# Optimization experiments

Hardware: AMD Instinct MI355X
Metric: run time of the kernel (lower is better)

## Reference

```python
import jax, jax.numpy as jnp
import numpy as np

B, SEQ, NV = 4, 1024, 32
PL, D, H, E_LAYERS, DFF = 16, 512, 8, 4, 2048
P = SEQ // PL  # 64 patches -> L = P*NV = 2048 tokens
WIN = 4
DH = D // H
SCALE = float(1.0 / np.sqrt(DH))


def layernorm(x, g, b):
    m = x.mean(-1, keepdims=True)
    v = jnp.var(x, axis=-1, keepdims=True)
    return (x - m) / jnp.sqrt(v + 1e-5) * g + b


def setup_inputs() -> dict:
    key = jax.random.key(0)
    ks = jax.random.split(key, 32)
    s = 0.02
    d = {}
    d['x_enc'] = jax.random.normal(ks[0], (B, SEQ, NV), jnp.float32)
    d['mask'] = jax.random.uniform(ks[1], (B, P, NV)) < 0.5  # mask_ratio=0.5
    d['W_embed'] = jax.random.normal(ks[2], (PL, D), jnp.float32) * s
    d['b_embed'] = jnp.zeros((D,), jnp.float32)
    per = lambda k, shp: jax.random.normal(k, (E_LAYERS,) + shp, jnp.float32) * s
    d['Wq'] = per(ks[3], (D, D)); d['bq'] = jnp.zeros((E_LAYERS, D))
    d['Wk'] = per(ks[4], (D, D)); d['bk'] = jnp.zeros((E_LAYERS, D))
    d['Wv'] = per(ks[5], (D, D)); d['bv'] = jnp.zeros((E_LAYERS, D))
    d['Wo'] = per(ks[6], (D, D)); d['bo'] = jnp.zeros((E_LAYERS, D))
    d['W1'] = per(ks[7], (D, DFF)); d['b1'] = jnp.zeros((E_LAYERS, DFF))
    d['W2'] = per(ks[8], (DFF, D)); d['b2'] = jnp.zeros((E_LAYERS, D))
    d['g1'] = jnp.ones((E_LAYERS, D)); d['be1'] = jnp.zeros((E_LAYERS, D))
    d['g2'] = jnp.ones((E_LAYERS, D)); d['be2'] = jnp.zeros((E_LAYERS, D))
    d['gf'] = jnp.ones((D,)); d['bf'] = jnp.zeros((D,))
    d['W_proj'] = jax.random.normal(ks[9], (D, PL), jnp.float32) * s
    d['b_proj'] = jnp.zeros((PL,), jnp.float32)
    return d


def reference(x_enc, mask, W_embed, b_embed, Wq, bq, Wk, bk, Wv, bv, Wo, bo,
              W1, b1, W2, b2, g1, be1, g2, be2, gf, bf, W_proj, b_proj):
    # instance norm over time (means detached, stdev differentiable as in torch)
    means = jax.lax.stop_gradient(x_enc.mean(1, keepdims=True))
    x = x_enc - means
    stdev = jnp.sqrt(jnp.var(x, axis=1, keepdims=True) + 1e-5)
    x = x / stdev
    # patchify: [B, P, NV, PL]
    patches = x[:, :P * PL, :].reshape(B, P, PL, NV).transpose(0, 1, 3, 2)
    emb = patches @ W_embed + b_embed                  # [B,P,NV,D]
    emb = jnp.where(mask[..., None], 0.0, emb)         # zero masked patches
    tok = emb.reshape(B, P * NV, D)                    # [B,L,D]
    # local/banded attention mask over patch index
    pid = jnp.arange(P * NV) // NV
    bad = jnp.abs(pid[:, None] - pid[None, :]) > WIN   # [L,L] True = masked
    for l in range(E_LAYERS):
        q = (tok @ Wq[l] + bq[l]).reshape(B, -1, H, DH)
        k = (tok @ Wk[l] + bk[l]).reshape(B, -1, H, DH)
        v = (tok @ Wv[l] + bv[l]).reshape(B, -1, H, DH)
        scores = jnp.einsum('blhe,bshe->bhls', q, k)
        scores = jnp.where(bad[None, None], -jnp.inf, scores)
        A = jax.nn.softmax(SCALE * scores, axis=-1)
        o = jnp.einsum('bhls,bshe->blhe', A, v).reshape(B, -1, D)
        tok = layernorm(tok + (o @ Wo[l] + bo[l]), g1[l], be1[l])
        y = jax.nn.gelu(tok @ W1[l] + b1[l], approximate=False) @ W2[l] + b2[l]
        tok = layernorm(tok + y, g2[l], be2[l])
    tok = layernorm(tok, gf, bf)
    enc = tok.reshape(B, P, NV, D)
    recon = enc @ W_proj + b_proj                      # [B,P,NV,PL]
    sc = stdev[:, 0, :][:, None, :, None]
    bi = means[:, 0, :][:, None, :, None]
    recon = recon * sc + bi
    target = patches * sc + bi
    mf = mask[..., None].astype(recon.dtype)
    denom = mf.sum() * PL
    denom = jnp.where(denom == 0, 1.0, denom)
    return (((recon - target) ** 2) * mf).sum() / denom
```

## Files before the change

### kernel.cpp

```cpp
#include <hip/hip_runtime.h>
#include <hip/hip_bf16.h>

#define DEV __device__ __forceinline__

namespace {

constexpr int Bn  = 4, SEQ = 1024, NV = 32, PL = 16, D = 512, H = 8, DFF = 2048;
constexpr int P   = SEQ / PL;
constexpr int L   = P * NV;
constexpr int M   = Bn * L;
constexpr int WIN = 4;

using short8   = __attribute__((ext_vector_type(8))) short;
using ushort8  = __attribute__((ext_vector_type(8))) unsigned short;
using float4v  = __attribute__((ext_vector_type(4))) float;

DEV float b2f(unsigned short u) { return __uint_as_float(((unsigned)u) << 16); }
DEV unsigned short f2b(float f) {
  unsigned fb = __float_as_uint(f);
  return (unsigned short)((fb + 0x7FFFu + ((fb >> 16) & 1u)) >> 16);
}
DEV unsigned short f2bt(float f) {
  return (unsigned short)(__float_as_uint(f) >> 16);
}
DEV float ldf(const void* p, size_t idx, int bf) {
  if (bf) return b2f(((const unsigned short*)p)[idx]);
  return ((const float*)p)[idx];
}
DEV void gll16(const void* gp, void* lp) {
  __builtin_amdgcn_global_load_lds(
      (const __attribute__((address_space(1))) void*)gp,
      (__attribute__((address_space(3))) void*)lp, 16, 0, 0);
}

__global__ void k_setup(const void* gf, const void* mask_raw, int* mask_i,
                        int* flags, float* scal) {
  __shared__ int s_gt1, s_oth, s_cnt;
  int tid = threadIdx.x;
  if (tid == 0) { s_gt1 = 0; s_oth = 0; s_cnt = 0; }
  __syncthreads();
  const unsigned* mw = (const unsigned*)mask_raw;
  int gt1 = 0, oth = 0;
  for (int i = tid; i < 2048; i += 256) {
    unsigned w = mw[i];
    if (w > 1u) { gt1 = 1; if (w != 0x3F800000u) oth = 1; }
  }
  if (gt1) atomicOr(&s_gt1, 1);
  if (oth) atomicOr(&s_oth, 1);
  __syncthreads();
  int fmt = (!s_gt1) ? 0 : (!s_oth ? 1 : 2);
  int cnt = 0;
  for (int i = tid; i < Bn * P * NV; i += 256) {
    int m;
    if (fmt == 0)      m = ((const int*)mask_raw)[i] != 0;
    else if (fmt == 1) m = ((const float*)mask_raw)[i] != 0.0f;
    else               m = ((const unsigned char*)mask_raw)[i] != 0;
    mask_i[i] = m; cnt += m;
  }
  atomicAdd(&s_cnt, cnt);
  __syncthreads();
  if (tid == 0) {
    unsigned w = *(const unsigned*)gf;
    flags[0] = ((w & 0xFFFFu) == 0x3F80u) ? 1 : 0;
    flags[1] = s_cnt;
    scal[0] = 0.f;
  }
}

__global__ void k_prep(const void* x, const void* bq, const void* bk,
                       const void* bv, const void* bo, const void* b1,
                       const void* b2, const void* gf, const void* bff,
                       const void* Wp, const void* bp, const int* flags,
                       float* means, float* stdev, float* biasf, float* lnw,
                       unsigned short* WpT) {
  int bf = flags[0];
  int tid = threadIdx.x;
  if (blockIdx.x < 32) {
    int bv_ = blockIdx.x * 4 + (tid >> 6);
    int b = bv_ >> 5, v = bv_ & 31;
    int lane = tid & 63;
    float s = 0.f, s2 = 0.f;
    for (int t = lane; t < SEQ; t += 64) {
      float val = ldf(x, (size_t)b * SEQ * NV + (size_t)t * NV + v, bf);
      s += val; s2 += val * val;
    }
    for (int off = 32; off; off >>= 1) {
      s += __shfl_xor(s, off); s2 += __shfl_xor(s2, off);
    }
    if (lane == 0) {
      float m = s / (float)SEQ;
      means[bv_] = m;
      stdev[bv_] = sqrtf(s2 / (float)SEQ - m * m + 1e-5f);
    }
    return;
  }
  int i = (blockIdx.x - 32) * 256 + tid;
  if (i < 18432) {
    int l = i / 4608, r = i % 4608;
    if (r < 1536) {
      float v = (r < 512) ? ldf(bq, l * 512 + r, bf)
              : (r < 1024) ? ldf(bk, l * 512 + r - 512, bf)
                           : ldf(bv, l * 512 + r - 1024, bf);
      biasf[l * 1536 + r] = v;
    } else if (r < 2048) {
      biasf[6144 + l * 512 + (r - 1536)] = ldf(bo, l * 512 + r - 1536, bf);
    } else if (r < 4096) {
      biasf[8192 + l * 2048 + (r - 2048)] = ldf(b1, l * 2048 + r - 2048, bf);
    } else {
      biasf[16384 + l * 512 + (r - 4096)] = ldf(b2, l * 512 + r - 4096, bf);
    }
  } else if (i < 19456) {
    int j = i - 18432;
    lnw[j] = (j < 512) ? ldf(gf, j, bf) : ldf(bff, j - 512, bf);
  } else if (i < 19472) {
    lnw[1024 + (i - 19456)] = ldf(bp, i - 19456, bf);
  } else if (i < 27664) {
    int j = i - 19472; int t = j >> 9, d = j & 511;
    WpT[j] = f2b(ldf(Wp, d * 16 + t, bf));
  }
}

__global__ void k_transpose_all(const void* Wq, const void* Wk, const void* Wv,
                                const void* Wo, const void* W1, const void* W2,
                                unsigned short* qkvT, unsigned short* WoT,
                                unsigned short* W1T, unsigned short* W2T,
                                const int* flags) {
  int bf = flags[0];
  int id = blockIdx.x;
  const void* src; unsigned short* dst;
  int Kd, Nd, l, n0, k0, dstOff = 0;
  size_t srcLS, dstLS;
  if (id < 4096) {
    int tensor = id >> 10, rem = id & 1023;
    l = rem >> 8; int t = rem & 255;
    n0 = (t & 15) * 32; k0 = (t >> 4) * 32;
    Kd = 512; Nd = 512; srcLS = 262144;
    if (tensor == 0)      { src = Wq; dst = qkvT; dstLS = 786432; dstOff = 0; }
    else if (tensor == 1) { src = Wk; dst = qkvT; dstLS = 786432; dstOff = 262144; }
    else if (tensor == 2) { src = Wv; dst = qkvT; dstLS = 786432; dstOff = 524288; }
    else                  { src = Wo; dst = WoT;  dstLS = 262144; }
  } else if (id < 8192) {
    int rem = id - 4096; l = rem >> 10; int t = rem & 1023;
    n0 = (t & 63) * 32; k0 = (t >> 6) * 32;
    Kd = 512; Nd = 2048; srcLS = 1048576; src = W1; dst = W1T; dstLS = 1048576;
  } else {
    int rem = id - 8192; l = rem >> 10; int t = rem & 1023;
    n0 = (t & 15) * 32; k0 = (t >> 4) * 32;
    Kd = 2048; Nd = 512; srcLS = 1048576; src = W2; dst = W2T; dstLS = 1048576;
  }
  int tx = threadIdx.x & 31, ty = threadIdx.x >> 5;
  __shared__ float tile[32][33];
  for (int rr = ty; rr < 32; rr += 8)
    tile[rr][tx] =
        ldf(src, (size_t)l * srcLS + (size_t)(k0 + rr) * Nd + n0 + tx, bf);
  __syncthreads();
  for (int rr = ty; rr < 32; rr += 8)
    dst[(size_t)l * dstLS + dstOff + (size_t)(n0 + rr) * Kd + k0 + tx] =
        f2b(tile[tx][rr]);
}

__global__ void k_embed(const void* x, const void* We, const void* be,
                        const int* flags, const int* mask_i,
                        const float* means, const float* stdev,
                        float* patches, unsigned short* tok) {
  int idx = blockIdx.x;
  int b = idx >> 11, pv = idx & 2047, p = pv >> 5, v = pv & 31;
  int bf = flags[0];
  __shared__ float pvs[PL];
  int tid = threadIdx.x;
  float m = means[b * NV + v], sd = stdev[b * NV + v];
  if (tid < PL) {
    float val =
        (ldf(x, (size_t)b * SEQ * NV + (size_t)(p * PL + tid) * NV + v, bf) -
         m) / sd;
    pvs[tid] = val;
    patches[(size_t)idx * PL + tid] = val;
  }
  __syncthreads();
  int masked = mask_i[idx];
  for (int d = tid; d < D; d += 128) {
    float acc = ldf(be, d, bf);
    for (int t = 0; t < PL; t++) acc += pvs[t] * ldf(We, t * D + d, bf);
    tok[(size_t)idx * D + d] = masked ? f2b(0.f) : f2b(acc);
  }
}

template <int BM, int BN, int WN>
__global__ __launch_bounds__(256) void k_gemm(
    const unsigned short* __restrict__ A, const unsigned short* __restrict__ W,
    const float* __restrict__ bias, const unsigned short* __restrict__ resid,
    unsigned short* __restrict__ C, unsigned short* __restrict__ vTp, int cs,
    int Kk, int act, int nbn) {
  constexpr int FI = 4, FJ = WN / 16, NWN = BN / WN;
  __shared__ __align__(16) char sm[BM * 128 + BN * 128];
  char* As = sm;
  char* Bs = sm + BM * 128;
  unsigned short* Cl = (unsigned short*)sm;
  int tid = threadIdx.x, lane = tid & 63, w = tid >> 6;
  int lane15 = lane & 15, q = lane >> 4;
  int wm = w / NWN, wn = w % NWN;
  int id = blockIdx.x;
  int xcd = id & 7, loc = id >> 3;
  int bn = (loc % nbn) * BN;
  int bm = (xcd * ((int)(gridDim.x >> 3) / nbn) + loc / nbn) * BM;
  int lrow = lane >> 3, lc = lane & 7;
  float4v acc[FI][FJ];
  for (int i = 0; i < FI; i++)
    for (int j = 0; j < FJ; j++) acc[i][j] = 0;
  for (int k0 = 0; k0 < Kk; k0 += 64) {
    if (k0) __syncthreads();
    for (int i = w; i < BM / 8; i += 4) {
      int row = i * 8 + lrow;
      gll16(A + (size_t)(bm + row) * Kk + k0 + ((lc ^ (row & 7)) << 3),
            As + i * 1024);
    }
    for (int i = w; i < BN / 8; i += 4) {
      int row = i * 8 + lrow;
      gll16(W + (size_t)(bn + row) * Kk + k0 + ((lc ^ (row & 7)) << 3),
            Bs + i * 1024);
    }
    __syncthreads();
    short8 a[2][FI], b[2][FJ];
    for (int h = 0; h < 2; h++) {
      for (int i = 0; i < FI; i++) {
        int rr = wm * 64 + i * 16 + lane15;
        a[h][i] =
            *(const short8*)(As + rr * 128 + (((h * 4 + q) ^ (rr & 7)) << 4));
      }
      for (int j = 0; j < FJ; j++) {
        int rr = wn * WN + j * 16 + lane15;
        b[h][j] =
            *(const short8*)(Bs + rr * 128 + (((h * 4 + q) ^ (rr & 7)) << 4));
      }
    }
    for (int h = 0; h < 2; h++)
      for (int i = 0; i < FI; i++)
        for (int j = 0; j < FJ; j++)
          acc[i][j] = __builtin_amdgcn_mfma_f32_16x16x32_bf16(
              a[h][i], b[h][j], acc[i][j], 0, 0, 0);
  }
  int vmode = (vTp != nullptr) && (bn >= 1024);
  float oscale = (vTp != nullptr && bn < 512) ? 0.125f : 1.0f;
  __syncthreads();
  for (int i = 0; i < FI; i++) {
    for (int j = 0; j < FJ; j++) {
      int col = wn * WN + j * 16 + lane15;
      float bv = bias[bn + col];
      for (int r = 0; r < 4; r++) {
        int row = wm * 64 + i * 16 + q * 4 + r;
        float cv = (acc[i][j][r] + bv) * oscale;
        if (act) {
          float t = cv * (1.5957692f + 0.0713548f * cv * cv);
          cv = cv / (1.f + __expf(-t));
        }
        if (!vmode)
          Cl[row * BN + (((col >> 3) ^ (row & 7)) << 3) + (col & 7)] = f2bt(cv);
        else
          Cl[col * BM + (((row >> 3) ^ (col & 7)) << 3) + (row & 7)] = f2bt(cv);
      }
    }
  }
  __syncthreads();
  if (!vmode) {
    constexpr int TOT = BM * BN / 8;
    for (int e = tid; e < TOT; e += 256) {
      int rr = e / (BN / 8), c8 = e % (BN / 8);
      ushort8 u = *(const ushort8*)(Cl + rr * BN + ((c8 ^ (rr & 7)) << 3));
      size_t off = (size_t)(bm + rr) * cs + bn + c8 * 8;
      if (resid) {
        ushort8 rv = *(const ushort8*)(resid + off);
        for (int t = 0; t < 8; t++) u[t] = f2bt(b2f(u[t]) + b2f(rv[t]));
      }
      *(ushort8*)(C + off) = u;
    }
  } else {
    constexpr int TOT = BM * BN / 8;
    for (int e = tid; e < TOT; e += 256) {
      int cc = e / (BM / 8), t8 = e % (BM / 8);
      ushort8 u = *(const ushort8*)(Cl + cc * BM + ((t8 ^ (cc & 7)) << 3));
      int hd = bn - 1024 + cc;
      int rowg = bm + t8 * 8;
      int bb = rowg >> 11, tokin = rowg & 2047;
      *(ushort8*)(vTp + ((size_t)(bb * 512 + hd)) * 2048 + tokin) = u;
    }
  }
}

#define G256_MM(QM, QN)                                                     \
  {                                                                         \
    __builtin_amdgcn_s_setprio(1);                                          \
    _Pragma("unroll") for (int kh = 0; kh < 2; ++kh) {                      \
      _Pragma("unroll") for (int mi = 0; mi < 2; ++mi) {                    \
        _Pragma("unroll") for (int ni = 0; ni < 4; ++ni) {                  \
          acc[QM][QN][mi][ni] = __builtin_amdgcn_mfma_f32_16x16x32_bf16(    \
              a[mi][kh], b[ni][kh], acc[QM][QN][mi][ni], 0, 0, 0);          \
        }                                                                   \
      }                                                                     \
    }                                                                       \
    __builtin_amdgcn_s_setprio(0);                                          \
  }

DEV short8 g256_frag(const char* base, int R, int kh, int q) {
  return *(const short8*)(base + R * 128 + (((kh * 4 + q) ^ (R & 7)) << 4));
}

DEV void g256_stage(const unsigned short* __restrict__ G, int row0, int Kk,
                    int tt, char* region, int Hh, int w, int lrow, int lc) {
#pragma unroll
  for (int j = 0; j < 2; ++j) {
    int R = Hh * 128 + j * 64 + w * 8 + lrow;
    gll16(G + (size_t)(row0 + R) * Kk + tt * 64 + ((lc ^ (R & 7)) << 3),
          region + (Hh * 128 + j * 64 + w * 8) * 128);
  }
}

__global__ __launch_bounds__(512) void k_gemm256(
    const unsigned short* __restrict__ A, const unsigned short* __restrict__ W,
    const float* __restrict__ bias, const unsigned short* __restrict__ resid,
    unsigned short* __restrict__ C, unsigned short* __restrict__ vTp, int cs,
    int Kk, int act, int nbn) {
  __shared__ __align__(16) char sm[131072];
  unsigned short* Cl = (unsigned short*)sm;
  int tid = threadIdx.x, lane = tid & 63, w = tid >> 6;
  int lane15 = lane & 15, q = lane >> 4;
  int lrow = lane >> 3, lc = lane & 7;
  int wr = (w & 3) * 32;
  int wc = (w >> 2) * 64;
  int id = blockIdx.x;
  int xcd = id & 7, loc = id >> 3;
  int bn = (loc % nbn) * 256;
  int bm = (xcd * ((int)(gridDim.x >> 3) / nbn) + loc / nbn) * 256;
  int NT = Kk >> 6;

  float4v acc[2][2][2][4];
#pragma unroll
  for (int i = 0; i < 2; i++)
#pragma unroll
    for (int j = 0; j < 2; j++)
#pragma unroll
      for (int mi = 0; mi < 2; mi++)
#pragma unroll
        for (int ni = 0; ni < 4; ni++) acc[i][j][mi][ni] = 0;

  {
    char* A0b = sm;
    char* B0b = sm + 32768;
    char* A1b = sm + 65536;
    char* B1b = sm + 98304;
    g256_stage(A, bm, Kk, 0, A0b, 0, w, lrow, lc);
    g256_stage(A, bm, Kk, 0, A0b, 1, w, lrow, lc);
    g256_stage(W, bn, Kk, 0, B0b, 0, w, lrow, lc);
    g256_stage(W, bn, Kk, 0, B0b, 1, w, lrow, lc);
    if (NT > 1) {
      g256_stage(A, bm, Kk, 1, A1b, 0, w, lrow, lc);
      g256_stage(W, bn, Kk, 1, B1b, 1, w, lrow, lc);
      g256_stage(A, bm, Kk, 1, A1b, 1, w, lrow, lc);
      asm volatile("s_waitcnt vmcnt(6)" ::: "memory");
    } else {
      asm volatile("s_waitcnt vmcnt(0)" ::: "memory");
    }
    __builtin_amdgcn_sched_barrier(0);
    __builtin_amdgcn_s_barrier();
  }

  for (int t = 0; t < NT; ++t) {
    char* Ac = sm + (t & 1) * 65536;
    char* Bc = Ac + 32768;
    char* An = sm + ((t + 1) & 1) * 65536;
    char* Bnx = An + 32768;
    short8 a[2][2], b[4][2];
#pragma unroll
    for (int mi = 0; mi < 2; ++mi)
#pragma unroll
      for (int kh = 0; kh < 2; ++kh)
        a[mi][kh] = g256_frag(Ac, wr + mi * 16 + lane15, kh, q);
#pragma unroll
    for (int ni = 0; ni < 4; ++ni)
#pragma unroll
      for (int kh = 0; kh < 2; ++kh)
        b[ni][kh] = g256_frag(Bc, wc + ni * 16 + lane15, kh, q);
    if (t + 1 < NT) g256_stage(W, bn, Kk, t + 1, Bnx, 0, w, lrow, lc);
    __builtin_amdgcn_s_barrier();
    G256_MM(0, 0);
    __builtin_amdgcn_s_barrier();
#pragma unroll
    for (int ni = 0; ni < 4; ++ni)
#pragma unroll
      for (int kh = 0; kh < 2; ++kh)
        b[ni][kh] = g256_frag(Bc, 128 + wc + ni * 16 + lane15, kh, q);
    if (t + 2 < NT) g256_stage(A, bm, Kk, t + 2, Ac, 0, w, lrow, lc);
    __builtin_amdgcn_s_barrier();
    G256_MM(0, 1);
    __builtin_amdgcn_s_barrier();
#pragma unroll
    for (int mi = 0; mi < 2; ++mi)
#pragma unroll
      for (int kh = 0; kh < 2; ++kh)
        a[mi][kh] = g256_frag(Ac, 128 + wr + mi * 16 + lane15, kh, q);
    if (t + 2 < NT) g256_stage(W, bn, Kk, t + 2, Bc, 1, w, lrow, lc);
    __builtin_amdgcn_s_barrier();
    G256_MM(1, 1);
    __builtin_amdgcn_s_barrier();
#pragma unroll
    for (int ni = 0; ni < 4; ++ni)
#pragma unroll
      for (int kh = 0; kh < 2; ++kh)
        b[ni][kh] = g256_frag(Bc, wc + ni * 16 + lane15, kh, q);
    if (t + 2 < NT) g256_stage(A, bm, Kk, t + 2, Ac, 1, w, lrow, lc);
    if (t + 2 < NT) {
      asm volatile("s_waitcnt vmcnt(6)" ::: "memory");
    } else if (t + 1 < NT) {
      asm volatile("s_waitcnt vmcnt(0)" ::: "memory");
    }
    __builtin_amdgcn_sched_barrier(0);
    __builtin_amdgcn_s_barrier();
    G256_MM(1, 0);
    __builtin_amdgcn_s_barrier();
  }

  int vmode = (vTp != nullptr) && (bn >= 1024);
  float oscale = (vTp != nullptr && bn < 512) ? 0.125f : 1.0f;
  __syncthreads();
#pragma unroll
  for (int QM = 0; QM < 2; QM++) {
#pragma unroll
    for (int QN = 0; QN < 2; QN++) {
#pragma unroll
      for (int mi = 0; mi < 2; mi++) {
#pragma unroll
        for (int ni = 0; ni < 4; ni++) {
          int col = QN * 128 + wc + ni * 16 + lane15;
          float bv = bias[bn + col];
#pragma unroll
          for (int r = 0; r < 4; r++) {
            int row = QM * 128 + wr + mi * 16 + q * 4 + r;
            float cv = (acc[QM][QN][mi][ni][r] + bv) * oscale;
            if (act) {
              float tt = cv * (1.5957692f + 0.0713548f * cv * cv);
              cv = cv / (1.f + __expf(-tt));
            }
            if (!vmode)
              Cl[row * 256 + (((col >> 3) ^ (row & 7)) << 3) + (col & 7)] =
                  f2bt(cv);
            else
              Cl[col * 256 + (((row >> 3) ^ (col & 7)) << 3) + (row & 7)] =
                  f2bt(cv);
          }
        }
      }
    }
  }
  __syncthreads();
  if (!vmode) {
    for (int e = tid; e < 8192; e += 512) {
      int rr = e >> 5, c8 = e & 31;
      ushort8 u = *(const ushort8*)(Cl + rr * 256 + ((c8 ^ (rr & 7)) << 3));
      size_t off = (size_t)(bm + rr) * cs + bn + c8 * 8;
      if (resid) {
        ushort8 rv = *(const ushort8*)(resid + off);
        for (int t = 0; t < 8; t++) u[t] = f2bt(b2f(u[t]) + b2f(rv[t]));
      }
      *(ushort8*)(C + off) = u;
    }
  } else {
    for (int e = tid; e < 8192; e += 512) {
      int cc = e >> 5, t8 = e & 31;
      ushort8 u = *(const ushort8*)(Cl + cc * 256 + ((t8 ^ (cc & 7)) << 3));
      int hd = bn - 1024 + cc;
      int rowg = bm + t8 * 8;
      int bb = rowg >> 11, tokin = rowg & 2047;
      *(ushort8*)(vTp + ((size_t)(bb * 512 + hd)) * 2048 + tokin) = u;
    }
  }
}

__global__ __launch_bounds__(256) void k_attn(
    const unsigned short* __restrict__ qk,
    const unsigned short* __restrict__ vT, unsigned short* __restrict__ o) {
  constexpr int SSTR = 304;
  __shared__ __align__(16) unsigned short S[32 * SSTR];
  int id = blockIdx.x;
  int xcd = id & 7, rr_ = id >> 3;
  int p = xcd * 8 + (rr_ & 7);
  int h = (rr_ >> 3) & 7;
  int b = rr_ >> 6;
  int tid = threadIdx.x, lane = tid & 63, w = tid >> 6;
  int lane15 = lane & 15, q = lane >> 4;
  int p0 = max(0, p - WIN), p1 = min(P - 1, p + WIN);
  int nk = (p1 - p0 + 1) * 32;
  int ntiles = nk >> 4;
  size_t base = (size_t)b * L;
  short8 aq[2][2];
  for (int m = 0; m < 2; m++) {
    const unsigned short* qrow =
        qk + (base + p * 32 + m * 16 + lane15) * 1024 + h * 64 + q * 8;
    aq[m][0] = *(const short8*)(qrow);
    aq[m][1] = *(const short8*)(qrow + 32);
  }
  const unsigned short* kbase =
      qk + (base + p0 * 32) * 1024 + 512 + h * 64 + q * 8;
  {
    int nt = w;
    const unsigned short* kr = kbase + (size_t)(nt * 16 + lane15) * 1024;
    short8 c0, c1, n0, n1;
    if (nt < ntiles) {
      c0 = *(const short8*)(kr);
      c1 = *(const short8*)(kr + 32);
    }
    if (nt + 4 < ntiles) {
      kr = kbase + (size_t)((nt + 4) * 16 + lane15) * 1024;
      n0 = *(const short8*)(kr);
      n1 = *(const short8*)(kr + 32);
    }
    for (; nt < ntiles; nt += 4) {
      short8 m0, m1;
      if (nt + 8 < ntiles) {
        kr = kbase + (size_t)((nt + 8) * 16 + lane15) * 1024;
        m0 = *(const short8*)(kr);
        m1 = *(const short8*)(kr + 32);
      }
      for (int m = 0; m < 2; m++) {
        float4v s4 = 0;
        s4 = __builtin_amdgcn_mfma_f32_16x16x32_bf16(aq[m][0], c0, s4, 0, 0, 0);
        s4 = __builtin_amdgcn_mfma_f32_16x16x32_bf16(aq[m][1], c1, s4, 0, 0, 0);
        for (int r = 0; r < 4; r++)
          S[(m * 16 + q * 4 + r) * SSTR + nt * 16 + lane15] = f2b(s4[r]);
      }
      c0 = n0; c1 = n1; n0 = m0; n1 = m1;
    }
  }
  __syncthreads();
  {
    int row = tid >> 3, c = tid & 7;
    ushort8 eb[5];
    float sum = 0.f;
    for (int k = 0; k < 5; k++) {
      int j0 = c * 8 + k * 64;
      if (j0 < nk) {
        ushort8 u = *(const ushort8*)(S + row * SSTR + j0);
        ushort8 e8;
        for (int t = 0; t < 8; t++) {
          float e = __expf(b2f(u[t]));
          sum += e;
          e8[t] = f2bt(e);
        }
        eb[k] = e8;
      }
    }
    for (int off = 1; off < 8; off <<= 1) sum += __shfl_xor(sum, off);
    float inv = 1.f / sum;
    for (int k = 0; k < 5; k++) {
      int j0 = c * 8 + k * 64;
      if (j0 < nk) {
        ushort8 e8 = eb[k], u;
        for (int t = 0; t < 8; t++) u[t] = f2bt(b2f(e8[t]) * inv);
        *(ushort8*)(S + row * SSTR + j0) = u;
      }
    }
  }
  __syncthreads();
  int nkt = nk >> 5;
  const unsigned short* vb =
      vT + (size_t)(b * 512 + h * 64 + w * 16 + lane15) * 2048 + p0 * 32 +
      q * 8;
  const unsigned short* pr0 = S + lane15 * SSTR + q * 8;
  const unsigned short* pr1 = S + (16 + lane15) * SSTR + q * 8;
  float4v oa0 = 0, oa1 = 0;
  short8 ap0 = *(const short8*)(pr0);
  short8 ap1 = *(const short8*)(pr1);
  short8 v0 = *(const short8*)(vb);
  for (int kt = 0; kt < nkt; kt++) {
    short8 a0N, a1N, v0N;
    if (kt + 1 < nkt) {
      a0N = *(const short8*)(pr0 + (kt + 1) * 32);
      a1N = *(const short8*)(pr1 + (kt + 1) * 32);
      v0N = *(const short8*)(vb + (kt + 1) * 32);
    }
    oa0 = __builtin_amdgcn_mfma_f32_16x16x32_bf16(ap0, v0, oa0, 0, 0, 0);
    oa1 = __builtin_amdgcn_mfma_f32_16x16x32_bf16(ap1, v0, oa1, 0, 0, 0);
    ap0 = a0N; ap1 = a1N; v0 = v0N;
  }
  __syncthreads();
  for (int r = 0; r < 4; r++) {
    S[(q * 4 + r) * 72 + w * 16 + lane15] = f2bt(oa0[r]);
    S[(16 + q * 4 + r) * 72 + w * 16 + lane15] = f2bt(oa1[r]);
  }
  __syncthreads();
  {
    int row = tid >> 3, c8 = tid & 7;
    ushort8 val = *(const ushort8*)(S + row * 72 + c8 * 8);
    *(ushort8*)(o + (base + p * 32 + row) * 512 + h * 64 + c8 * 8) = val;
  }
}

__global__ void k_ln(const unsigned short* __restrict__ x, const void* g,
                     const void* bta, unsigned short* __restrict__ out,
                     const int* flags, int goff) {
  int bf = flags[0];
  int row = blockIdx.x * 4 + (threadIdx.x >> 6);
  int lane = threadIdx.x & 63;
  ushort8 u = *(const ushort8*)(x + (size_t)row * D + lane * 8);
  float v[8]; float s = 0.f, s2 = 0.f;
  for (int t = 0; t < 8; t++) {
    v[t] = b2f(u[t]); s += v[t]; s2 += v[t] * v[t];
  }
  for (int off = 32; off; off >>= 1) {
    s += __shfl_xor(s, off); s2 += __shfl_xor(s2, off);
  }
  float m = s / (float)D;
  float inv = rsqrtf(s2 / (float)D - m * m + 1e-5f);
  ushort8 ou;
  for (int t = 0; t < 8; t++) {
    int c = lane * 8 + t;
    ou[t] = f2b((v[t] - m) * inv * ldf(g, goff + c, bf) + ldf(bta, goff + c, bf));
  }
  *(ushort8*)(out + (size_t)row * D + lane * 8) = ou;
}

__global__ __launch_bounds__(128) void k_lnloss(
    const unsigned short* __restrict__ tok, const float* __restrict__ lnw,
    const unsigned short* __restrict__ WpT, const float* __restrict__ patches,
    const float* __restrict__ stdev, const int* __restrict__ mask_i,
    float* scal) {
  constexpr int RS = 520;
  __shared__ __align__(16) unsigned short As[32 * RS];
  __shared__ __align__(16) unsigned short Bs[16 * RS];
  int bpI = blockIdx.x; int b = bpI >> 6, p = bpI & 63;
  int tid = threadIdx.x;
  int row = tid >> 2, cg = tid & 3;
  size_t tokbase = (size_t)(b * L + p * 32);
  float s = 0.f, s2 = 0.f;
  for (int i = 0; i < 16; i++) {
    int c = cg + i * 4;
    ushort8 u = *(const ushort8*)(tok + (tokbase + row) * D + c * 8);
    for (int t = 0; t < 8; t++) { float v = b2f(u[t]); s += v; s2 += v * v; }
  }
  s += __shfl_xor(s, 1); s += __shfl_xor(s, 2);
  s2 += __shfl_xor(s2, 1); s2 += __shfl_xor(s2, 2);
  float m = s / (float)D;
  float inv = rsqrtf(s2 / (float)D - m * m + 1e-5f);
  for (int i = 0; i < 16; i++) {
    int c = cg + i * 4;
    ushort8 u = *(const ushort8*)(tok + (tokbase + row) * D + c * 8);
    ushort8 o;
    for (int t = 0; t < 8; t++) {
      int col = c * 8 + t;
      o[t] = f2b((b2f(u[t]) - m) * inv * lnw[col] + lnw[512 + col]);
    }
    *(ushort8*)(As + row * RS + c * 8) = o;
  }
  for (int e = tid; e < 16 * 64; e += 128) {
    int r = e >> 6, c = e & 63;
    *(ushort8*)(Bs + r * RS + c * 8) = *(const ushort8*)(WpT + r * 512 + c * 8);
  }
  __syncthreads();
  int w = tid >> 6, lane = tid & 63, lane15 = lane & 15, q = lane >> 4;
  float4v acc = 0;
  for (int kt = 0; kt < 16; kt++) {
    short8 a = *(const short8*)(As + (w * 16 + lane15) * RS + kt * 32 + q * 8);
    short8 bfr = *(const short8*)(Bs + lane15 * RS + kt * 32 + q * 8);
    acc = __builtin_amdgcn_mfma_f32_16x16x32_bf16(a, bfr, acc, 0, 0, 0);
  }
  float local = 0.f;
  int t = lane15;
  for (int r = 0; r < 4; r++) {
    int v = w * 16 + q * 4 + r;
    int tokidx = b * 2048 + p * 32 + v;
    if (mask_i[tokidx]) {
      float recon = acc[r] + lnw[1024 + t];
      float diff = recon - patches[(size_t)tokidx * 16 + t];
      float sc = stdev[b * 32 + v];
      local += sc * sc * diff * diff;
    }
  }
  for (int off = 32; off; off >>= 1) local += __shfl_xor(local, off);
  if (lane == 0) atomicAdd(&scal[0], local);
}

__global__ void k_final(const float* scal, const int* flags, unsigned* out) {
  float denom = (float)flags[1] * (float)PL;
  if (denom == 0.f) denom = 1.f;
  float loss = scal[0] / denom;
  unsigned fb = __float_as_uint(loss);
  unsigned u = (fb + 0x7FFFu + ((fb >> 16) & 1u)) >> 16;
  out[0] = (u << 16) | u;
}

}

extern "C" void kernel_launch(void* const* d_in, const int* in_sizes, int n_in,
                              void* d_out, int out_size, void* d_ws,
                              size_t ws_size, hipStream_t stream) {
  const void* x_enc = d_in[0];
  const void* maskp = d_in[1];
  const void* We = d_in[2];  const void* be_ = d_in[3];
  const void* Wq = d_in[4];  const void* bq = d_in[5];
  const void* Wk = d_in[6];  const void* bk = d_in[7];
  const void* Wv = d_in[8];  const void* bv = d_in[9];
  const void* Wo = d_in[10]; const void* bo_ = d_in[11];
  const void* W1 = d_in[12]; const void* b1 = d_in[13];
  const void* W2 = d_in[14]; const void* b2 = d_in[15];
  const void* g1 = d_in[16]; const void* be1 = d_in[17];
  const void* g2 = d_in[18]; const void* be2 = d_in[19];
  const void* gf = d_in[20]; const void* bff = d_in[21];
  const void* Wp = d_in[22]; const void* bp = d_in[23];

  constexpr size_t MB = 1u << 20;
  char* w = (char*)d_ws;
  int*   mask_i  = (int*)w;
  int*   flags   = (int*)(w + 32768);
  float* scal    = (float*)(w + 32896);
  float* means   = (float*)(w + 33024);
  float* stdev   = (float*)(w + 33600);
  float* biasf   = (float*)(w + 36864);
  float* lnw     = (float*)(w + 114688);
  float* patches = (float*)(w + 131072);
  unsigned short* WpT = (unsigned short*)(w + 655360);
  unsigned short* qkvT = (unsigned short*)(w + 1 * MB);
  unsigned short* WoT  = (unsigned short*)(w + 7 * MB);
  unsigned short* W1T  = (unsigned short*)(w + 9 * MB);
  unsigned short* W2T  = (unsigned short*)(w + 17 * MB);
  unsigned short* tok  = (unsigned short*)(w + 25 * MB);
  unsigned short* tmp  = (unsigned short*)(w + 33 * MB);
  unsigned short* ob   = (unsigned short*)(w + 41 * MB);
  unsigned short* qk   = (unsigned short*)(w + 49 * MB);
  unsigned short* vTb  = (unsigned short*)(w + 73 * MB);
  unsigned short* hidden = ob;

  k_setup<<<1, 256, 0, stream>>>(gf, maskp, mask_i, flags, scal);
  k_prep<<<141, 256, 0, stream>>>(x_enc, bq, bk, bv, bo_, b1, b2, gf, bff, Wp,
                                  bp, flags, means, stdev, biasf, lnw, WpT);
  k_transpose_all<<<12288, 256, 0, stream>>>(Wq, Wk, Wv, Wo, W1, W2, qkvT, WoT,
                                             W1T, W2T, flags);
  k_embed<<<M, 128, 0, stream>>>(x_enc, We, be_, flags, mask_i, means, stdev,
                                 patches, tok);
  for (int l = 0; l < 4; l++) {
    k_gemm256<<<192, 512, 0, stream>>>(
        tok, qkvT + (size_t)l * 786432, biasf + l * 1536, nullptr, qk, vTb,
        1024, 512, 0, 6);
    k_attn<<<2048, 256, 0, stream>>>(qk, vTb, ob);
    k_gemm<64, 64, 16><<<1024, 256, 0, stream>>>(
        ob, WoT + (size_t)l * 262144, biasf + 6144 + l * 512, tok, tmp,
        nullptr, 512, 512, 0, 8);
    k_ln<<<M / 4, 256, 0, stream>>>(tmp, g1, be1, tok, flags, l * 512);
    k_gemm256<<<256, 512, 0, stream>>>(
        tok, W1T + (size_t)l * 1048576, biasf + 8192 + l * 2048, nullptr,
        hidden, nullptr, 2048, 512, 1, 8);
    k_gemm<64, 64, 16><<<1024, 256, 0, stream>>>(
        hidden, W2T + (size_t)l * 1048576, biasf + 16384 + l * 512, tok, tmp,
        nullptr, 512, 2048, 0, 8);
    k_ln<<<M / 4, 256, 0, stream>>>(tmp, g2, be2, tok, flags, l * 512);
  }
  k_lnloss<<<Bn * P, 128, 0, stream>>>(tok, lnw, WpT, patches, stdev, mask_i,
                                       scal);
  k_final<<<1, 1, 0, stream>>>(scal, flags, (unsigned*)d_out);
}
```

Before: 892.7 us.

## Reorder 256-tile GEMM quadrant schedule with finer vmcnt waits; use smaller-tile QKV GEMM

The 256x256 GEMM main loop now runs its four MFMA quadrants in the order (0,1),(1,1),(1,0),(0,0). It keeps two A fragment sets so that one B fragment load serves two quadrants, which cuts the LDS fragment reloads and the barrier pairs per k-step. The s_waitcnt counts are retuned for the new load order, and the kernel now declares launch bounds of 2 blocks per CU. Separately, the QKV projection moves from the 256-tile kernel to the 128x64 k_gemm with 1536 blocks, which gives more parallelism for that smaller GEMM. The risks are register pressure from the extra fragment registers and wrong vmcnt counts causing races.

```diff
diff --git a/kernel.cpp b/kernel.cpp
--- a/kernel.cpp
+++ b/kernel.cpp
@@ -286,18 +286,18 @@
   }
 }
 
-#define G256_MM(QM, QN)                                                     \
+#define VW(n) asm volatile("s_waitcnt vmcnt(" #n ")" ::: "memory")
+
+#define G256_MM(QM, QN, AR, BR)                                             \
   {                                                                         \
-    __builtin_amdgcn_s_setprio(1);                                          \
     _Pragma("unroll") for (int kh = 0; kh < 2; ++kh) {                      \
       _Pragma("unroll") for (int mi = 0; mi < 2; ++mi) {                    \
         _Pragma("unroll") for (int ni = 0; ni < 4; ++ni) {                  \
           acc[QM][QN][mi][ni] = __builtin_amdgcn_mfma_f32_16x16x32_bf16(    \
-              a[mi][kh], b[ni][kh], acc[QM][QN][mi][ni], 0, 0, 0);          \
+              AR[mi][kh], BR[ni][kh], acc[QM][QN][mi][ni], 0, 0, 0);        \
         }                                                                   \
       }                                                                     \
     }                                                                       \
-    __builtin_amdgcn_s_setprio(0);                                          \
   }
 
 DEV short8 g256_frag(const char* base, int R, int kh, int q) {
@@ -314,7 +314,7 @@
   }
 }
 
-__global__ __launch_bounds__(512) void k_gemm256(
+__global__ __launch_bounds__(512, 2) void k_gemm256(
     const unsigned short* __restrict__ A, const unsigned short* __restrict__ W,
     const float* __restrict__ bias, const unsigned short* __restrict__ resid,
     unsigned short* __restrict__ C, unsigned short* __restrict__ vTp, int cs,
@@ -343,21 +343,17 @@
         for (int ni = 0; ni < 4; ni++) acc[i][j][mi][ni] = 0;
 
   {
-    char* A0b = sm;
-    char* B0b = sm + 32768;
-    char* A1b = sm + 65536;
-    char* B1b = sm + 98304;
-    g256_stage(A, bm, Kk, 0, A0b, 0, w, lrow, lc);
-    g256_stage(A, bm, Kk, 0, A0b, 1, w, lrow, lc);
-    g256_stage(W, bn, Kk, 0, B0b, 0, w, lrow, lc);
-    g256_stage(W, bn, Kk, 0, B0b, 1, w, lrow, lc);
+    g256_stage(A, bm, Kk, 0, sm, 0, w, lrow, lc);
+    g256_stage(W, bn, Kk, 0, sm + 32768, 1, w, lrow, lc);
+    g256_stage(A, bm, Kk, 0, sm, 1, w, lrow, lc);
+    g256_stage(W, bn, Kk, 0, sm + 32768, 0, w, lrow, lc);
     if (NT > 1) {
-      g256_stage(A, bm, Kk, 1, A1b, 0, w, lrow, lc);
-      g256_stage(W, bn, Kk, 1, B1b, 1, w, lrow, lc);
-      g256_stage(A, bm, Kk, 1, A1b, 1, w, lrow, lc);
-      asm volatile("s_waitcnt vmcnt(6)" ::: "memory");
+      g256_stage(A, bm, Kk, 1, sm + 65536, 0, w, lrow, lc);
+      g256_stage(W, bn, Kk, 1, sm + 98304, 1, w, lrow, lc);
+      g256_stage(A, bm, Kk, 1, sm + 65536, 1, w, lrow, lc);
+      VW(10);
     } else {
-      asm volatile("s_waitcnt vmcnt(0)" ::: "memory");
+      VW(4);
     }
     __builtin_amdgcn_sched_barrier(0);
     __builtin_amdgcn_s_barrier();
@@ -368,53 +364,56 @@
     char* Bc = Ac + 32768;
     char* An = sm + ((t + 1) & 1) * 65536;
     char* Bnx = An + 32768;
-    short8 a[2][2], b[4][2];
+    short8 a0[2][2], a1[2][2], bb[4][2];
 #pragma unroll
     for (int mi = 0; mi < 2; ++mi)
 #pragma unroll
       for (int kh = 0; kh < 2; ++kh)
-        a[mi][kh] = g256_frag(Ac, wr + mi * 16 + lane15, kh, q);
+        a0[mi][kh] = g256_frag(Ac, wr + mi * 16 + lane15, kh, q);
 #pragma unroll
     for (int ni = 0; ni < 4; ++ni)
 #pragma unroll
       for (int kh = 0; kh < 2; ++kh)
-        b[ni][kh] = g256_frag(Bc, wc + ni * 16 + lane15, kh, q);
+        bb[ni][kh] = g256_frag(Bc, 128 + wc + ni * 16 + lane15, kh, q);
     if (t + 1 < NT) g256_stage(W, bn, Kk, t + 1, Bnx, 0, w, lrow, lc);
     __builtin_amdgcn_s_barrier();
-    G256_MM(0, 0);
-    __builtin_amdgcn_s_barrier();
-#pragma unroll
-    for (int ni = 0; ni < 4; ++ni)
-#pragma unroll
-      for (int kh = 0; kh < 2; ++kh)
-        b[ni][kh] = g256_frag(Bc, 128 + wc + ni * 16 + lane15, kh, q);
-    if (t + 2 < NT) g256_stage(A, bm, Kk, t + 2, Ac, 0, w, lrow, lc);
-    __builtin_amdgcn_s_barrier();
-    G256_MM(0, 1);
-    __builtin_amdgcn_s_barrier();
-#pragma unroll
-    for (int mi = 0; mi < 2; ++mi)
-#pragma unroll
-      for (int kh = 0; kh < 2; ++kh)
-        a[mi][kh] = g256_frag(Ac, 128 + wr + mi * 16 + lane15, kh, q);
-    if (t + 2 < NT) g256_stage(W, bn, Kk, t + 2, Bc, 1, w, lrow, lc);
-    __builtin_amdgcn_s_barrier();
-    G256_MM(1, 1);
-    __builtin_amdgcn_s_barrier();
-#pragma unroll
-    for (int ni = 0; ni < 4; ++ni)
-#pragma unroll
-      for (int kh = 0; kh < 2; ++kh)
-        b[ni][kh] = g256_frag(Bc, wc + ni * 16 + lane15, kh, q);
-    if (t + 2 < NT) g256_stage(A, bm, Kk, t + 2, Ac, 1, w, lrow, lc);
-    if (t + 2 < NT) {
-      asm volatile("s_waitcnt vmcnt(6)" ::: "memory");
-    } else if (t + 1 < NT) {
-      asm volatile("s_waitcnt vmcnt(0)" ::: "memory");
-    }
+    __builtin_amdgcn_s_setprio(1);
+    G256_MM(0, 1, a0, bb);
+    __builtin_amdgcn_s_setprio(0);
+    if (t + 1 < NT) { VW(10); } else { VW(2); }
     __builtin_amdgcn_sched_barrier(0);
     __builtin_amdgcn_s_barrier();
-    G256_MM(1, 0);
+#pragma unroll
+    for (int mi = 0; mi < 2; ++mi)
+#pragma unroll
+      for (int kh = 0; kh < 2; ++kh)
+        a1[mi][kh] = g256_frag(Ac, 128 + wr + mi * 16 + lane15, kh, q);
+    if (t + 2 < NT) {
+      g256_stage(A, bm, Kk, t + 2, Ac, 0, w, lrow, lc);
+      g256_stage(W, bn, Kk, t + 2, Bc, 1, w, lrow, lc);
+    }
+    __builtin_amdgcn_s_barrier();
+    __builtin_amdgcn_s_setprio(1);
+    G256_MM(1, 1, a1, bb);
+    __builtin_amdgcn_s_setprio(0);
+    if (t + 2 < NT) { VW(12); } else if (t + 1 < NT) { VW(8); } else { VW(0); }
+    __builtin_amdgcn_sched_barrier(0);
+    __builtin_amdgcn_s_barrier();
+#pragma unroll
+    for (int ni = 0; ni < 4; ++ni)
+#pragma unroll
+      for (int kh = 0; kh < 2; ++kh)
+        bb[ni][kh] = g256_frag(Bc, wc + ni * 16 + lane15, kh, q);
+    if (t + 2 < NT) g256_stage(A, bm, Kk, t + 2, Ac, 1, w, lrow, lc);
+    __builtin_amdgcn_s_barrier();
+    __builtin_amdgcn_s_setprio(1);
+    G256_MM(1, 0, a1, bb);
+    G256_MM(0, 0, a0, bb);
+    __builtin_amdgcn_s_setprio(0);
+    if (t + 1 < NT) {
+      if (t + 2 < NT) { VW(10); } else { VW(4); }
+      __builtin_amdgcn_sched_barrier(0);
+    }
     __builtin_amdgcn_s_barrier();
   }
 
@@ -468,8 +467,8 @@
       ushort8 u = *(const ushort8*)(Cl + cc * 256 + ((t8 ^ (cc & 7)) << 3));
       int hd = bn - 1024 + cc;
       int rowg = bm + t8 * 8;
-      int bb = rowg >> 11, tokin = rowg & 2047;
-      *(ushort8*)(vTp + ((size_t)(bb * 512 + hd)) * 2048 + tokin) = u;
+      int bb2 = rowg >> 11, tokin = rowg & 2047;
+      *(ushort8*)(vTp + ((size_t)(bb2 * 512 + hd)) * 2048 + tokin) = u;
     }
   }
 }
@@ -735,9 +734,9 @@
   k_embed<<<M, 128, 0, stream>>>(x_enc, We, be_, flags, mask_i, means, stdev,
                                  patches, tok);
   for (int l = 0; l < 4; l++) {
-    k_gemm256<<<192, 512, 0, stream>>>(
+    k_gemm<128, 64, 32><<<1536, 256, 0, stream>>>(
         tok, qkvT + (size_t)l * 786432, biasf + l * 1536, nullptr, qk, vTb,
-        1024, 512, 0, 6);
+        1024, 512, 0, 24);
     k_attn<<<2048, 256, 0, stream>>>(qk, vTb, ob);
     k_gemm<64, 64, 16><<<1024, 256, 0, stream>>>(
         ob, WoT + (size_t)l * 262144, biasf + 6144 + l * 512, tok, tmp,
```

Measured after the change: 876.3 us. About the same (-1.8%).
